# Performance work log

Hardware: AMD Instinct MI355X
Metric: run time of the kernel (lower is better)

## Reference

```python
import jax, jax.numpy as jnp
import numpy as np

B, N, D_IN, H = 1024, 512, 30, 64


def setup_inputs() -> dict:
    key = jax.random.key(0)
    ks = jax.random.split(key, 9)
    s_fc = 1.0 / np.sqrt(D_IN)
    s_rnn = 1.0 / np.sqrt(H)
    return {
        "x": jax.random.normal(ks[0], (B, N, D_IN), dtype=jnp.float32),
        "W_fc": jax.random.uniform(ks[1], (H, D_IN), jnp.float32, -s_fc, s_fc),
        "b_fc": jax.random.uniform(ks[2], (H,), jnp.float32, -s_fc, s_fc),
        "W_ih": jax.random.uniform(ks[3], (4 * H, H), jnp.float32, -s_rnn, s_rnn),
        "W_hh": jax.random.uniform(ks[4], (4 * H, H), jnp.float32, -s_rnn, s_rnn),
        "b_ih": jax.random.uniform(ks[5], (4 * H,), jnp.float32, -s_rnn, s_rnn),
        "b_hh": jax.random.uniform(ks[6], (4 * H,), jnp.float32, -s_rnn, s_rnn),
        "W_last": jax.random.uniform(ks[7], (1, H), jnp.float32, -s_rnn, s_rnn),
        "b_last": jax.random.uniform(ks[8], (1,), jnp.float32, -s_rnn, s_rnn),
    }


def _lstm(xg, W_hh):
    # xg: (B, N, 4H) precomputed input-side gate preactivations (biases included)
    # PyTorch gate order: i, f, g, o
    Hh = W_hh.shape[1]
    B_ = xg.shape[0]
    h0 = jnp.zeros((B_, Hh), xg.dtype)
    c0 = jnp.zeros((B_, Hh), xg.dtype)

    def step(carry, xg_t):
        h, c = carry
        g = xg_t + h @ W_hh.T  # (B, 4H)
        i, f, gg, o = jnp.split(g, 4, axis=-1)
        i = jax.nn.sigmoid(i)
        f = jax.nn.sigmoid(f)
        gg = jnp.tanh(gg)
        o = jax.nn.sigmoid(o)
        c = f * c + i * gg
        h = o * jnp.tanh(c)
        return (h, c), h

    _, hs = jax.lax.scan(step, (h0, c0), jnp.swapaxes(xg, 0, 1))  # (N, B, H)
    return jnp.swapaxes(hs, 0, 1)  # (B, N, H)


def reference(x, W_fc, b_fc, W_ih, W_hh, b_ih, b_hh, W_last, b_last):
    hid = x @ W_fc.T + b_fc                  # (B, N, H)
    xg = hid @ W_ih.T + (b_ih + b_hh)        # (B, N, 4H), input-side precompute
    hs = _lstm(xg, W_hh)                     # (B, N, H)
    # dropout is identity in eval / dropout_ratio=0
    logits = hs @ W_last.T + b_last          # (B, N, 1)
    w = jax.nn.softmax(logits, axis=1)
    return jnp.squeeze(w, axis=-1)           # (B, N)
```

## Files before the change

kernel.cpp:

```cpp
#include <hip/hip_runtime.h>

#define B_SZ  1024
#define NSEQ  512
#define D_INP 30
#define H     64
#define MB    4
#define TCH   8
#define L2E   1.4426950408889634f

typedef short s16x8 __attribute__((ext_vector_type(8)));
typedef float f32x4 __attribute__((ext_vector_type(4)));

#if __has_builtin(__builtin_amdgcn_exp2f)
#define EXP2(x) __builtin_amdgcn_exp2f(x)
#else
#define EXP2(x) exp2f(x)
#endif

__device__ __forceinline__ float rcp_f(float v) { return __builtin_amdgcn_rcpf(v); }

__device__ __forceinline__ f32x4 mfma16(s16x8 a, s16x8 b, f32x4 c) {
  return __builtin_amdgcn_mfma_f32_16x16x32_bf16(a, b, c, 0, 0, 0);
}

__device__ __forceinline__ short bf16_rne(float f) {
  unsigned u = __float_as_uint(f);
  unsigned r = (u + 0x7FFFu + ((u >> 16) & 1u)) >> 16;
  return (short)r;
}

__device__ __forceinline__ s16x8 rne8(const float* f) {
  s16x8 o;
#pragma unroll
  for (int i = 0; i < 8; ++i) o[i] = bf16_rne(f[i]);
  return o;
}

__device__ __forceinline__ void split8(const float* f, s16x8& hi, s16x8& lo) {
#pragma unroll
  for (int i = 0; i < 8; ++i) {
    unsigned ub = __float_as_uint(f[i]);
    hi[i] = (short)(ub >> 16);
    float hf = __uint_as_float(ub & 0xFFFF0000u);
    float lf = f[i] - hf;
    lo[i] = (short)(__float_as_uint(lf) >> 16);
  }
}

__device__ __forceinline__ void wg_barrier() {
  asm volatile("s_waitcnt lgkmcnt(0)" ::: "memory");
  __builtin_amdgcn_s_barrier();
  asm volatile("" ::: "memory");
}

__global__ __launch_bounds__(256) void prep_kernel(
    const float* __restrict__ W_fc, const float* __restrict__ b_fc,
    const float* __restrict__ W_ih, const float* __restrict__ b_ih,
    const float* __restrict__ b_hh,
    float* __restrict__ wsW, float* __restrict__ wsB) {
  __shared__ float fc[H * D_INP];
  __shared__ float bfc[H];
  const int u = threadIdx.x;
  for (int i = u; i < H * D_INP; i += 256) fc[i] = W_fc[i];
  if (u < H) bfc[u] = b_fc[u];
  __syncthreads();

  float wih[H];
#pragma unroll
  for (int i = 0; i < H; ++i) wih[i] = W_ih[u * H + i];

  for (int k = 0; k < D_INP; ++k) {
    float s = 0.f;
#pragma unroll
    for (int i = 0; i < H; ++i) s = fmaf(wih[i], fc[i * D_INP + k], s);
    wsW[u * 32 + k] = s;
  }
  wsW[u * 32 + 30] = 0.f;
  wsW[u * 32 + 31] = 0.f;

  float bb = b_ih[u] + b_hh[u];
#pragma unroll
  for (int i = 0; i < H; ++i) bb = fmaf(wih[i], bfc[i], bb);
  wsB[u] = bb;
}

__global__ __launch_bounds__(512, 2) void lstm_mfma(
    const float* __restrict__ x, const float* __restrict__ W_hh,
    const float* __restrict__ wsW, const float* __restrict__ wsB,
    const float* __restrict__ W_last, float* __restrict__ out) {

  __shared__ short xa[2][TCH][64][8];
  __shared__ short hpl[2][16][72];
  __shared__ float logitsT[NSEQ + 1][MB];

  const int u   = threadIdx.x;
  const int w   = u >> 6;
  const int l   = u & 63;
  const int low = l & 15;
  const int q   = l >> 4;
  const int b0  = blockIdx.x * MB;
  const bool isS = (w >= 4);
  const int cw  = w & 3;

  s16x8 whh[4][2], wcb[4];
  float xb[4];
  s16x8 wl_h[2], wl_l[2];

  if (!isS) {
    float tmp[8];
#pragma unroll
    for (int g2 = 0; g2 < 4; ++g2) {
      const int n = 64 * g2 + 16 * cw + low;
      const float sc = (g2 == 2) ? (2.0f * L2E) : L2E;
#pragma unroll
      for (int kt = 0; kt < 2; ++kt) {
        const float* p = W_hh + n * H + kt * 32 + q * 8;
#pragma unroll
        for (int j = 0; j < 8; ++j) tmp[j] = p[j] * sc;
        whh[g2][kt] = rne8(tmp);
      }
      const float* pw = wsW + n * 32 + q * 8;
#pragma unroll
      for (int j = 0; j < 8; ++j) tmp[j] = pw[j] * sc;
      wcb[g2] = rne8(tmp);
      xb[g2] = wsB[n] * sc;
    }
  } else {
#pragma unroll
    for (int kt = 0; kt < 2; ++kt) {
      float tmp[8];
#pragma unroll
      for (int j = 0; j < 8; ++j)
        tmp[j] = (low == 0) ? W_last[kt * 32 + q * 8 + j] : 0.0f;
      split8(tmp, wl_h[kt], wl_l[kt]);
    }
  }

  for (int i = u; i < 2 * TCH * 64 * 8 / 2; i += 512) ((int*)xa)[i] = 0;
  for (int i = u; i < 2 * 16 * 72 / 2; i += 512) ((int*)hpl)[i] = 0;
  __syncthreads();

  const int srow = l & 15, sq = l >> 4;
  const bool sact = (srow & 3) == 0;
  const float* xrow = x + (size_t)(b0 + (srow >> 2)) * NSEQ * D_INP + sq * 8;
  float pf0[8], pf1[8];
  auto ld8 = [&](const float* p, float* pf) {
    float2 v0 = *(const float2*)(p);
    float2 v1 = *(const float2*)(p + 2);
    float2 v2 = *(const float2*)(p + 4);
    float2 v3 = (sq < 3) ? *(const float2*)(p + 6) : make_float2(0.f, 0.f);
    pf[0] = v0.x; pf[1] = v0.y; pf[2] = v1.x; pf[3] = v1.y;
    pf[4] = v2.x; pf[5] = v2.y; pf[6] = v3.x; pf[7] = v3.y;
  };
  auto stage_load = [&](int t0) {
    const float* p = xrow + (size_t)(t0 + 2 * cw) * D_INP;
    ld8(p, pf0);
    ld8(p + D_INP, pf1);
  };
  auto stage_write = [&](int buf) {
    if (sact) {
      *(s16x8*)&xa[buf][2 * cw][l][0] = rne8(pf0);
      *(s16x8*)&xa[buf][2 * cw + 1][l][0] = rne8(pf1);
    }
  };

  if (isS) { stage_load(0); stage_write(0); }
  __syncthreads();

  f32x4 xacc[4];
  if (!isS) {
    s16x8 xah = *(const s16x8*)&xa[0][0][l][0];
#pragma unroll
    for (int g2 = 0; g2 < 4; ++g2) {
      f32x4 a = {xb[g2], xb[g2], xb[g2], xb[g2]};
      xacc[g2] = mfma16(xah, wcb[g2], a);
    }
  }

  float cst = 0.f;

  for (int t = 0; t < NSEQ; ++t) {
    const int tt = t & (TCH - 1);
    const int cb = (t >> 3) & 1;
    if (!isS) {
      const short* hp = &hpl[(t + 1) & 1][low][0];
      s16x8 ah0 = *(const s16x8*)(hp + q * 8);
      s16x8 ah1 = *(const s16x8*)(hp + 32 + q * 8);

      f32x4 acc[4];
#pragma unroll
      for (int g2 = 0; g2 < 4; ++g2) acc[g2] = mfma16(ah0, whh[g2][0], xacc[g2]);
#pragma unroll
      for (int g2 = 0; g2 < 4; ++g2) acc[g2] = mfma16(ah1, whh[g2][1], acc[g2]);

      if (t + 1 < NSEQ) {
        const int t1 = t + 1;
        s16x8 xah = *(const s16x8*)&xa[(t1 >> 3) & 1][t1 & 7][l][0];
#pragma unroll
        for (int g2 = 0; g2 < 4; ++g2) {
          f32x4 a = {xb[g2], xb[g2], xb[g2], xb[g2]};
          xacc[g2] = mfma16(xah, wcb[g2], a);
        }
      }

      float gi = rcp_f(1.0f + EXP2(-acc[0][0]));
      float gf = rcp_f(1.0f + EXP2(-acc[1][0]));
      float gg = 1.0f - 2.0f * rcp_f(1.0f + EXP2(acc[2][0]));
      float go = rcp_f(1.0f + EXP2(-acc[3][0]));
      float cc = fmaf(gf, cst, gi * gg);
      cst = cc;
      float h = go * (1.0f - 2.0f * rcp_f(1.0f + EXP2(cc * (2.0f * L2E))));
      hpl[t & 1][q * 4][16 * cw + low] = bf16_rne(h);
    } else {
      if (cw == (t & 3)) {
        const short* hp = &hpl[(t + 1) & 1][low][0];
        s16x8 ah0 = *(const s16x8*)(hp + q * 8);
        s16x8 ah1 = *(const s16x8*)(hp + 32 + q * 8);
        f32x4 aL = {0.f, 0.f, 0.f, 0.f};
        aL = mfma16(ah0, wl_h[0], aL);
        aL = mfma16(ah1, wl_h[1], aL);
        f32x4 bL = {0.f, 0.f, 0.f, 0.f};
        bL = mfma16(ah0, wl_l[0], bL);
        bL = mfma16(ah1, wl_l[1], bL);
        aL = aL + bL;
        if (low == 0) logitsT[t][q] = aL[0];
      }
      if (tt == 0 && t + TCH < NSEQ) stage_load(t + TCH);
      if (tt == 4 && t + 4 < NSEQ) stage_write(cb ^ 1);
    }
    wg_barrier();
  }

  if (w == 4) {
    const short* hp = &hpl[1][low][0];
    s16x8 ah0 = *(const s16x8*)(hp + q * 8);
    s16x8 ah1 = *(const s16x8*)(hp + 32 + q * 8);
    f32x4 aL = {0.f, 0.f, 0.f, 0.f};
    aL = mfma16(ah0, wl_h[0], aL);
    aL = mfma16(ah1, wl_h[1], aL);
    f32x4 bL = {0.f, 0.f, 0.f, 0.f};
    bL = mfma16(ah0, wl_l[0], bL);
    bL = mfma16(ah1, wl_l[1], bL);
    aL = aL + bL;
    if (low == 0) logitsT[NSEQ][q] = aL[0];
  }
  __syncthreads();

  if (u < 16 * MB) {
    const int m = u >> 4, li = u & 15;
    float lv[32];
    float mx = -3.0e38f;
#pragma unroll
    for (int s = 0; s < 32; ++s) {
      lv[s] = logitsT[1 + li + 16 * s][m];
      mx = fmaxf(mx, lv[s]);
    }
#pragma unroll
    for (int d = 1; d < 16; d <<= 1) mx = fmaxf(mx, __shfl_xor(mx, d, 16));
    float sum = 0.f;
#pragma unroll
    for (int s = 0; s < 32; ++s) { lv[s] = __expf(lv[s] - mx); sum += lv[s]; }
#pragma unroll
    for (int d = 1; d < 16; d <<= 1) sum += __shfl_xor(sum, d, 16);
    float inv = 1.0f / sum;
#pragma unroll
    for (int s = 0; s < 32; ++s)
      out[(size_t)(b0 + m) * NSEQ + li + 16 * s] = lv[s] * inv;
  }
}

extern "C" void kernel_launch(void* const* d_in, const int* in_sizes, int n_in,
                              void* d_out, int out_size, void* d_ws, size_t ws_size,
                              hipStream_t stream) {
  const float* x      = (const float*)d_in[0];
  const float* W_fc   = (const float*)d_in[1];
  const float* b_fc   = (const float*)d_in[2];
  const float* W_ih   = (const float*)d_in[3];
  const float* W_hh   = (const float*)d_in[4];
  const float* b_ih   = (const float*)d_in[5];
  const float* b_hh   = (const float*)d_in[6];
  const float* W_last = (const float*)d_in[7];

  float* out = (float*)d_out;
  float* wsW = (float*)d_ws;
  float* wsB = wsW + 256 * 32;

  prep_kernel<<<1, 256, 0, stream>>>(W_fc, b_fc, W_ih, b_ih, b_hh, wsW, wsB);
  lstm_mfma<<<B_SZ / MB, 512, 0, stream>>>(x, W_hh, wsW, wsB, W_last, out);
}
```

Before: 263.8 us.

## Process eight batch rows per block as two interleaved LSTM groups

Each block now handles eight sequences as two independent groups. Their recurrent MFMA chains and gate activations are interleaved within one timestep, giving more instruction-level parallelism and using the staged x-fragment rows more fully. The price is half as many blocks, which leaves many CUs idle, and roughly twice the serial work per step in each wave. The weight-prep kernel is also split across eight blocks instead of one.

```diff
diff --git a/kernel.cpp b/kernel.cpp
--- a/kernel.cpp
+++ b/kernel.cpp
@@ -4,7 +4,8 @@
 #define NSEQ  512
 #define D_INP 30
 #define H     64
-#define MB    4
+#define MB    8
+#define NG    2
 #define TCH   8
 #define L2E   1.4426950408889634f
 
@@ -65,23 +66,26 @@
   if (u < H) bfc[u] = b_fc[u];
   __syncthreads();
 
-  float wih[H];
-#pragma unroll
-  for (int i = 0; i < H; ++i) wih[i] = W_ih[u * H + i];
-
-  for (int k = 0; k < D_INP; ++k) {
-    float s = 0.f;
-#pragma unroll
-    for (int i = 0; i < H; ++i) s = fmaf(wih[i], fc[i * D_INP + k], s);
-    wsW[u * 32 + k] = s;
-  }
-  wsW[u * 32 + 30] = 0.f;
-  wsW[u * 32 + 31] = 0.f;
-
-  float bb = b_ih[u] + b_hh[u];
-#pragma unroll
-  for (int i = 0; i < H; ++i) bb = fmaf(wih[i], bfc[i], bb);
-  wsB[u] = bb;
+  const int n = blockIdx.x * 32 + u;
+  if (u < 32) {
+    float wih[H];
+#pragma unroll
+    for (int i = 0; i < H; ++i) wih[i] = W_ih[n * H + i];
+
+    for (int k = 0; k < D_INP; ++k) {
+      float s = 0.f;
+#pragma unroll
+      for (int i = 0; i < H; ++i) s = fmaf(wih[i], fc[i * D_INP + k], s);
+      wsW[n * 32 + k] = s;
+    }
+    wsW[n * 32 + 30] = 0.f;
+    wsW[n * 32 + 31] = 0.f;
+
+    float bb = b_ih[n] + b_hh[n];
+#pragma unroll
+    for (int i = 0; i < H; ++i) bb = fmaf(wih[i], bfc[i], bb);
+    wsB[n] = bb;
+  }
 }
 
 __global__ __launch_bounds__(512, 2) void lstm_mfma(
@@ -90,7 +94,7 @@
     const float* __restrict__ W_last, float* __restrict__ out) {
 
   __shared__ short xa[2][TCH][64][8];
-  __shared__ short hpl[2][16][72];
+  __shared__ short hpl[NG][2][16][72];
   __shared__ float logitsT[NSEQ + 1][MB];
 
   const int u   = threadIdx.x;
@@ -136,13 +140,11 @@
     }
   }
 
-  for (int i = u; i < 2 * TCH * 64 * 8 / 2; i += 512) ((int*)xa)[i] = 0;
-  for (int i = u; i < 2 * 16 * 72 / 2; i += 512) ((int*)hpl)[i] = 0;
-  __syncthreads();
+  for (int i = u; i < NG * 2 * 16 * 72 / 2; i += 512) ((int*)hpl)[i] = 0;
 
   const int srow = l & 15, sq = l >> 4;
-  const bool sact = (srow & 3) == 0;
-  const float* xrow = x + (size_t)(b0 + (srow >> 2)) * NSEQ * D_INP + sq * 8;
+  const bool sact = (srow < MB);
+  const float* xrow = x + (size_t)(b0 + (srow & (MB - 1))) * NSEQ * D_INP + sq * 8;
   float pf0[8], pf1[8];
   auto ld8 = [&](const float* p, float* pf) {
     float2 v0 = *(const float2*)(p);
@@ -167,53 +169,71 @@
   if (isS) { stage_load(0); stage_write(0); }
   __syncthreads();
 
-  f32x4 xacc[4];
+  auto xfrag = [&](int g, int t) -> s16x8 {
+    return *(const s16x8*)&xa[(t >> 3) & 1][t & 7][(q << 4) | (4 * g + (low >> 2))][0];
+  };
+
+  f32x4 xaccA[4], xaccB[4];
   if (!isS) {
-    s16x8 xah = *(const s16x8*)&xa[0][0][l][0];
+    s16x8 xA = xfrag(0, 0), xB = xfrag(1, 0);
 #pragma unroll
     for (int g2 = 0; g2 < 4; ++g2) {
       f32x4 a = {xb[g2], xb[g2], xb[g2], xb[g2]};
-      xacc[g2] = mfma16(xah, wcb[g2], a);
-    }
-  }
-
-  float cst = 0.f;
+      xaccA[g2] = mfma16(xA, wcb[g2], a);
+      xaccB[g2] = mfma16(xB, wcb[g2], a);
+    }
+  }
+
+  float cstA = 0.f, cstB = 0.f;
+
+#define ACT_H(ACC0, ACC1, ACC2, ACC3, CST, GRP)                              \
+  {                                                                          \
+    float gi = rcp_f(1.0f + EXP2(-(ACC0)));                                  \
+    float gf = rcp_f(1.0f + EXP2(-(ACC1)));                                  \
+    float gg = 1.0f - 2.0f * rcp_f(1.0f + EXP2((ACC2)));                     \
+    float go = rcp_f(1.0f + EXP2(-(ACC3)));                                  \
+    float cc = fmaf(gf, CST, gi * gg);                                       \
+    CST = cc;                                                                \
+    float hh2 = go * (1.0f - 2.0f * rcp_f(1.0f + EXP2(cc * (2.0f * L2E)))); \
+    hpl[GRP][t & 1][q * 4][16 * cw + low] = bf16_rne(hh2);                   \
+  }
 
   for (int t = 0; t < NSEQ; ++t) {
     const int tt = t & (TCH - 1);
     const int cb = (t >> 3) & 1;
     if (!isS) {
-      const short* hp = &hpl[(t + 1) & 1][low][0];
-      s16x8 ah0 = *(const s16x8*)(hp + q * 8);
-      s16x8 ah1 = *(const s16x8*)(hp + 32 + q * 8);
-
-      f32x4 acc[4];
-#pragma unroll
-      for (int g2 = 0; g2 < 4; ++g2) acc[g2] = mfma16(ah0, whh[g2][0], xacc[g2]);
-#pragma unroll
-      for (int g2 = 0; g2 < 4; ++g2) acc[g2] = mfma16(ah1, whh[g2][1], acc[g2]);
+      const short* hpA = &hpl[0][(t + 1) & 1][low][0];
+      const short* hpB = &hpl[1][(t + 1) & 1][low][0];
+      s16x8 a0A = *(const s16x8*)(hpA + q * 8);
+      s16x8 a1A = *(const s16x8*)(hpA + 32 + q * 8);
+      s16x8 a0B = *(const s16x8*)(hpB + q * 8);
+      s16x8 a1B = *(const s16x8*)(hpB + 32 + q * 8);
+
+      f32x4 accA[4], accB[4];
+#pragma unroll
+      for (int g2 = 0; g2 < 4; ++g2) accA[g2] = mfma16(a0A, whh[g2][0], xaccA[g2]);
+#pragma unroll
+      for (int g2 = 0; g2 < 4; ++g2) accA[g2] = mfma16(a1A, whh[g2][1], accA[g2]);
+#pragma unroll
+      for (int g2 = 0; g2 < 4; ++g2) accB[g2] = mfma16(a0B, whh[g2][0], xaccB[g2]);
+#pragma unroll
+      for (int g2 = 0; g2 < 4; ++g2) accB[g2] = mfma16(a1B, whh[g2][1], accB[g2]);
 
       if (t + 1 < NSEQ) {
-        const int t1 = t + 1;
-        s16x8 xah = *(const s16x8*)&xa[(t1 >> 3) & 1][t1 & 7][l][0];
+        s16x8 xA = xfrag(0, t + 1), xB = xfrag(1, t + 1);
 #pragma unroll
         for (int g2 = 0; g2 < 4; ++g2) {
           f32x4 a = {xb[g2], xb[g2], xb[g2], xb[g2]};
-          xacc[g2] = mfma16(xah, wcb[g2], a);
+          xaccA[g2] = mfma16(xA, wcb[g2], a);
+          xaccB[g2] = mfma16(xB, wcb[g2], a);
         }
       }
 
-      float gi = rcp_f(1.0f + EXP2(-acc[0][0]));
-      float gf = rcp_f(1.0f + EXP2(-acc[1][0]));
-      float gg = 1.0f - 2.0f * rcp_f(1.0f + EXP2(acc[2][0]));
-      float go = rcp_f(1.0f + EXP2(-acc[3][0]));
-      float cc = fmaf(gf, cst, gi * gg);
-      cst = cc;
-      float h = go * (1.0f - 2.0f * rcp_f(1.0f + EXP2(cc * (2.0f * L2E))));
-      hpl[t & 1][q * 4][16 * cw + low] = bf16_rne(h);
+      ACT_H(accA[0][0], accA[1][0], accA[2][0], accA[3][0], cstA, 0);
+      ACT_H(accB[0][0], accB[1][0], accB[2][0], accB[3][0], cstB, 1);
     } else {
-      if (cw == (t & 3)) {
-        const short* hp = &hpl[(t + 1) & 1][low][0];
+      if (cw < NG) {
+        const short* hp = &hpl[cw][(t + 1) & 1][low][0];
         s16x8 ah0 = *(const s16x8*)(hp + q * 8);
         s16x8 ah1 = *(const s16x8*)(hp + 32 + q * 8);
         f32x4 aL = {0.f, 0.f, 0.f, 0.f};
@@ -223,16 +243,18 @@
         bL = mfma16(ah0, wl_l[0], bL);
         bL = mfma16(ah1, wl_l[1], bL);
         aL = aL + bL;
-        if (low == 0) logitsT[t][q] = aL[0];
+        if (low == 0) logitsT[t][4 * cw + q] = aL[0];
       }
       if (tt == 0 && t + TCH < NSEQ) stage_load(t + TCH);
       if (tt == 4 && t + 4 < NSEQ) stage_write(cb ^ 1);
     }
     wg_barrier();
   }
-
-  if (w == 4) {
-    const short* hp = &hpl[1][low][0];
+#undef ACT_H
+
+  if (w == 4 || w == 5) {
+    const int g = w - 4;
+    const short* hp = &hpl[g][1][low][0];
     s16x8 ah0 = *(const s16x8*)(hp + q * 8);
     s16x8 ah1 = *(const s16x8*)(hp + 32 + q * 8);
     f32x4 aL = {0.f, 0.f, 0.f, 0.f};
@@ -242,7 +264,7 @@
     bL = mfma16(ah0, wl_l[0], bL);
     bL = mfma16(ah1, wl_l[1], bL);
     aL = aL + bL;
-    if (low == 0) logitsT[NSEQ][q] = aL[0];
+    if (low == 0) logitsT[NSEQ][4 * g + q] = aL[0];
   }
   __syncthreads();
 
@@ -285,6 +307,6 @@
   float* wsW = (float*)d_ws;
   float* wsB = wsW + 256 * 32;
 
-  prep_kernel<<<1, 256, 0, stream>>>(W_fc, b_fc, W_ih, b_ih, b_hh, wsW, wsB);
+  prep_kernel<<<8, 256, 0, stream>>>(W_fc, b_fc, W_ih, b_ih, b_hh, wsW, wsB);
   lstm_mfma<<<B_SZ / MB, 512, 0, stream>>>(x, W_hh, wsW, wsB, W_last, out);
 }
```

New measurement: 319.4 us. 1.21x slower.
